# Performance work log

Measured on AMD Instinct MI355X. Metric: run time of the kernel, lower is better.

Reference implementation:

```python
import jax, jax.numpy as jnp
import numpy as np

N = 80000          # nodes
E = 1280000        # edges (~avg degree 16)
D_IN = 64          # Lorentz ambient dim (1 time + 63 spatial feature dims)
D_HID = 64
EPS = 1e-8


def _lorentz_inner(x):
    # <x,x>_L = -x0^2 + ||x_space||^2  (keepdims)
    return -x[:, :1] * x[:, :1] + jnp.sum(x[:, 1:] * x[:, 1:], axis=-1, keepdims=True)


def _to_manifold(s):
    # scale so that <s,s>_L = -1 (curvature c=1 hyperboloid)
    denom = jnp.sqrt(jnp.clip(jnp.abs(_lorentz_inner(s)), EPS))
    return s / denom


def _lorentz_linear(x, W, b, log_scale, nonlin=None):
    # HyboNet LorentzLinear: dense map, then rebuild a valid hyperboloid point
    if nonlin is not None:
        x = nonlin(x)
    h = x @ W.T + b
    time = jax.nn.sigmoid(h[:, :1]) * jnp.exp(log_scale) + 1.1
    space = h[:, 1:]
    sq = jnp.clip(jnp.sum(space * space, axis=-1, keepdims=True), EPS)
    scale = (time * time - 1.0) / sq
    return jnp.concatenate([time, space * jnp.sqrt(scale)], axis=-1)


def _agg(h, src, dst, w):
    # sparse adjacency aggregation (spmm) + Lorentz centroid normalization
    s = jax.ops.segment_sum(w[:, None] * h[src], dst, num_segments=N)
    return _to_manifold(s)


def setup_inputs() -> dict:
    key = jax.random.key(0)
    ks = jax.random.split(key, 6)
    x = jax.random.normal(ks[0], (N, D_IN - 1), jnp.float32)
    edge_index = jax.random.randint(ks[1], (2, E), 0, N, dtype=jnp.int32)
    edge_weight = jax.random.uniform(ks[2], (E,), jnp.float32)
    W1 = jax.random.normal(ks[3], (D_HID, D_IN), jnp.float32) * 0.02
    b1 = jnp.zeros((D_HID,), jnp.float32)
    s1 = jnp.asarray(np.log(10.0), jnp.float32)   # LorentzLinear scale param (log-space)
    W2 = jax.random.normal(ks[4], (D_HID, D_HID), jnp.float32) * 0.02
    b2 = jnp.zeros((D_HID,), jnp.float32)
    s2 = jnp.asarray(np.log(10.0), jnp.float32)
    return dict(x=x, edge_index=edge_index, edge_weight=edge_weight,
                W1=W1, b1=b1, s1=s1, W2=W2, b2=b2, s2=s2)


def reference(x, edge_index, edge_weight, W1, b1, s1, W2, b2, s2):
    src, dst = edge_index[0], edge_index[1]
    n = x.shape[0]
    # lift to Lorentz tangent space at origin: prepend zero time coord
    # (proj_tan0 is then a no-op since time component is already 0)
    u_space = x                                             # [N, D_IN-1]
    # expmap0 (c=1): [cosh(||u||), sinh(||u||) * u/||u||]
    nrm = jnp.clip(jnp.linalg.norm(u_space, axis=-1, keepdims=True), EPS)
    p_space = jnp.sinh(nrm) * u_space / nrm
    # projx: recompute time coord from spatial part, x0 = sqrt(1 + ||x_s||^2)
    p_time = jnp.sqrt(1.0 + jnp.sum(p_space * p_space, axis=-1, keepdims=True))
    p = jnp.concatenate([p_time, p_space], axis=1)          # [N, D_IN]
    # conv1 (no nonlin) and conv2 (relu) = LorentzLinear + Lorentz aggregation
    h1 = _agg(_lorentz_linear(p, W1, b1, s1), src, dst, edge_weight)
    h2 = _agg(_lorentz_linear(h1, W2, b2, s2, nonlin=jax.nn.relu), src, dst, edge_weight)
    # LResNet hyperbolic residual: Lorentz-normalized sum of the two points
    return _to_manifold(h1 + h2)
```

## Files before the change

kernel.cpp:

```cpp
#include <hip/hip_runtime.h>
#include <hip/hip_bf16.h>

#define D 64
#define EPS 1e-8f
#define BSH 10
#define BNODES (1 << BSH)
#define ABLK 4096

typedef __attribute__((ext_vector_type(8))) short bf16x8;
typedef __attribute__((ext_vector_type(4))) float f32x4;

__device__ __forceinline__ float wave_sum64(float v) {
    #pragma unroll
    for (int d = 1; d < 64; d <<= 1) v += __shfl_xor(v, d);
    return v;
}

__device__ __forceinline__ unsigned short f2bf_rn(float f) {
    unsigned u = __float_as_uint(f);
    return (unsigned short)((u + 0x7FFFu + ((u >> 16) & 1u)) >> 16);
}

__device__ __forceinline__ void split8(float4 a, float4 b, bf16x8& h, bf16x8& l) {
    float f[8] = {a.x, a.y, a.z, a.w, b.x, b.y, b.z, b.w};
    #pragma unroll
    for (int i = 0; i < 8; ++i) {
        unsigned u = __float_as_uint(f[i]);
        float hf = __uint_as_float(u & 0xFFFF0000u);
        unsigned lu = __float_as_uint(f[i] - hf);
        h[i] = (short)(u >> 16);
        l[i] = (short)(lu >> 16);
    }
}

__global__ __launch_bounds__(256) void k_bcount(const int* __restrict__ dst,
                                                int* __restrict__ bcnt,
                                                int e, int nbuck) {
    __shared__ int cnt[128];
    int tid = threadIdx.x;
    if (tid < 128) cnt[tid] = 0;
    __syncthreads();
    int i0 = blockIdx.x * 1024 + tid;
    #pragma unroll
    for (int u = 0; u < 4; ++u) {
        int i = i0 + u * 256;
        if (i < e) atomicAdd(&cnt[dst[i] >> BSH], 1);
    }
    __syncthreads();
    if (tid < nbuck && cnt[tid]) atomicAdd(&bcnt[tid], cnt[tid]);
}

__global__ __launch_bounds__(128) void k_bscan(const int* __restrict__ bcnt,
                                               int* __restrict__ bstart,
                                               int* __restrict__ gcur,
                                               int* __restrict__ off,
                                               int n, int e, int nbuck) {
    __shared__ int sm[128];
    int tid = threadIdx.x;
    int v = (tid < nbuck) ? bcnt[tid] : 0;
    sm[tid] = v;
    __syncthreads();
    #pragma unroll
    for (int d = 1; d < 128; d <<= 1) {
        int t = (tid >= d) ? sm[tid - d] : 0;
        __syncthreads();
        sm[tid] += t;
        __syncthreads();
    }
    int excl = sm[tid] - v;
    if (tid < nbuck) { bstart[tid] = excl; gcur[tid] = excl; }
    if (tid == 0) { bstart[nbuck] = e; off[n] = e; }
}

__global__ __launch_bounds__(256) void k_bucketA(const int* __restrict__ src,
                                                 const int* __restrict__ dst,
                                                 const float* __restrict__ w,
                                                 int* __restrict__ gcur,
                                                 unsigned long long* __restrict__ tmp,
                                                 int e, int nbuck) {
    __shared__ int cnt[128];
    __shared__ int base[128];
    int tid = threadIdx.x;
    if (tid < 128) cnt[tid] = 0;
    __syncthreads();
    int i0 = blockIdx.x * ABLK + tid;
    int bkt[16], rnk[16];
    #pragma unroll
    for (int u = 0; u < 16; ++u) {
        int i = i0 + u * 256;
        if (i < e) {
            int b = dst[i] >> BSH;
            bkt[u] = b;
            rnk[u] = atomicAdd(&cnt[b], 1);
        }
    }
    __syncthreads();
    if (tid < 128) {
        int c = cnt[tid];
        base[tid] = c ? atomicAdd(&gcur[tid], c) : 0;
    }
    __syncthreads();
    #pragma unroll
    for (int u = 0; u < 16; ++u) {
        int i = i0 + u * 256;
        if (i < e) {
            unsigned long long pk =
                ((unsigned long long)__float_as_uint(w[i]) << 32)
                | (unsigned int)(src[i] | ((dst[i] & (BNODES - 1)) << 20));
            tmp[base[bkt[u]] + rnk[u]] = pk;
        }
    }
}

__global__ __launch_bounds__(1024) void k_bucketB(const unsigned long long* __restrict__ tmp,
                                                  const int* __restrict__ bstart,
                                                  int* __restrict__ off,
                                                  unsigned long long* __restrict__ epack,
                                                  int n) {
    __shared__ int cur[BNODES];
    __shared__ int sm[BNODES];
    int b = blockIdx.x;
    int v0 = b << BSH;
    int nv = min(BNODES, n - v0);
    int tid = threadIdx.x;
    cur[tid] = 0;
    __syncthreads();
    int s0 = bstart[b], s1 = bstart[b + 1];
    for (int i = s0 + tid; i < s1; i += 1024)
        atomicAdd(&cur[((unsigned)tmp[i] >> 20) & (BNODES - 1)], 1);
    __syncthreads();
    int v = cur[tid];
    sm[tid] = v;
    __syncthreads();
    #pragma unroll
    for (int d = 1; d < BNODES; d <<= 1) {
        int t = (tid >= d) ? sm[tid - d] : 0;
        __syncthreads();
        sm[tid] += t;
        __syncthreads();
    }
    int node_off = s0 + sm[tid] - v;
    if (tid < nv) off[v0 + tid] = node_off;
    cur[tid] = node_off;
    __syncthreads();
    for (int i = s0 + tid; i < s1; i += 1024) {
        unsigned long long pk = tmp[i];
        int dl = ((unsigned)pk >> 20) & (BNODES - 1);
        int pos = atomicAdd(&cur[dl], 1);
        __builtin_nontemporal_store(pk & 0xFFFFFFFFC00FFFFFULL, &epack[pos]);
    }
}

__global__ __launch_bounds__(256) void k_embed(const float* __restrict__ x,
                                               float* __restrict__ P, int n) {
    int lane = threadIdx.x & 63, wv = threadIdx.x >> 6;
    int q = lane >> 4, sub = lane & 15;
    int node = blockIdx.x * 16 + wv * 4 + q;
    if (node >= n) return;
    const float* xr = x + (size_t)node * 63;
    float v0 = 0.f, v1, v2, v3;
    if (sub == 0) {
        v1 = xr[0]; v2 = xr[1]; v3 = xr[2];
    } else {
        int b = sub * 4 - 1;
        v0 = xr[b]; v1 = xr[b + 1]; v2 = xr[b + 2]; v3 = xr[b + 3];
    }
    float s = v0 * v0 + v1 * v1 + v2 * v2 + v3 * v3;
    #pragma unroll
    for (int d2 = 1; d2 < 16; d2 <<= 1) s += __shfl_xor(s, d2);
    float nrm = fmaxf(sqrtf(s), EPS);
    float sh = sinhf(nrm);
    float k = sh / nrm;
    float4 r;
    if (sub == 0) r = make_float4(sqrtf(1.f + sh * sh), k * v1, k * v2, k * v3);
    else          r = make_float4(k * v0, k * v1, k * v2, k * v3);
    *(float4*)(P + (size_t)node * 64 + sub * 4) = r;
}

template <int RELU>
__global__ __launch_bounds__(256) void k_lin_mfma(const float* __restrict__ tbl,
                                                  const float* __restrict__ W,
                                                  const float* __restrict__ bias,
                                                  const float* __restrict__ sc,
                                                  unsigned short* __restrict__ out, int n) {
    int lane = threadIdx.x & 63, wv = threadIdx.x >> 6;
    int col = lane & 15, grp = lane >> 4;
    int node0 = blockIdx.x * 64 + wv * 16;
    if (node0 >= n) return;

    float es = expf(sc[0]);

    bf16x8 wh[2][4], wl[2][4];
    #pragma unroll
    for (int s = 0; s < 2; ++s)
        #pragma unroll
        for (int t = 0; t < 4; ++t) {
            const float* wp = W + (t * 16 + col) * 64 + s * 32 + grp * 8;
            split8(*(const float4*)wp, *(const float4*)(wp + 4), wh[s][t], wl[s][t]);
        }

    f32x4 acc[4];
    #pragma unroll
    for (int t = 0; t < 4; ++t) {
        float bv = bias[t * 16 + col];
        acc[t] = (f32x4){bv, bv, bv, bv};
    }

    int arow = node0 + col;
    if (arow >= n) arow = n - 1;
    #pragma unroll
    for (int s = 0; s < 2; ++s) {
        const float* ap = tbl + (size_t)arow * 64 + s * 32 + grp * 8;
        float4 a0 = *(const float4*)ap;
        float4 a1 = *(const float4*)(ap + 4);
        if (RELU) {
            a0.x = fmaxf(a0.x, 0.f); a0.y = fmaxf(a0.y, 0.f);
            a0.z = fmaxf(a0.z, 0.f); a0.w = fmaxf(a0.w, 0.f);
            a1.x = fmaxf(a1.x, 0.f); a1.y = fmaxf(a1.y, 0.f);
            a1.z = fmaxf(a1.z, 0.f); a1.w = fmaxf(a1.w, 0.f);
        }
        bf16x8 ah, al;
        split8(a0, a1, ah, al);
        #pragma unroll
        for (int t = 0; t < 4; ++t) {
            acc[t] = __builtin_amdgcn_mfma_f32_16x16x32_bf16(ah, wh[s][t], acc[t], 0, 0, 0);
            acc[t] = __builtin_amdgcn_mfma_f32_16x16x32_bf16(al, wh[s][t], acc[t], 0, 0, 0);
            acc[t] = __builtin_amdgcn_mfma_f32_16x16x32_bf16(ah, wl[s][t], acc[t], 0, 0, 0);
        }
    }

    float tot[4];
    #pragma unroll
    for (int r = 0; r < 4; ++r) {
        float s = 0.f;
        #pragma unroll
        for (int t = 0; t < 4; ++t) s += acc[t][r] * acc[t][r];
        tot[r] = s;
    }
    #pragma unroll
    for (int d2 = 1; d2 < 16; d2 <<= 1) {
        #pragma unroll
        for (int r = 0; r < 4; ++r) tot[r] += __shfl_xor(tot[r], d2);
    }
    float tm[4], rs[4];
    #pragma unroll
    for (int r = 0; r < 4; ++r) {
        float h0 = __shfl(acc[0][r], lane & 48);
        tm[r] = es / (1.f + expf(-h0)) + 1.1f;
        float sq = fmaxf(tot[r] - h0 * h0, EPS);
        rs[r] = sqrtf((tm[r] * tm[r] - 1.f) / sq);
    }
    #pragma unroll
    for (int t = 0; t < 4; ++t) {
        #pragma unroll
        for (int r = 0; r < 4; ++r) {
            int row = node0 + grp * 4 + r;
            if (row < n) {
                int j = t * 16 + col;
                float v = (j == 0) ? tm[r] : acc[t][r] * rs[r];
                out[(size_t)row * 64 + j] = f2bf_rn(v);
            }
        }
    }
}

template <int FINAL>
__global__ __launch_bounds__(256) void k_agg(const unsigned short* __restrict__ t,
                                             const int* __restrict__ off,
                                             const unsigned long long* __restrict__ epack,
                                             const float* __restrict__ h1,
                                             float* __restrict__ out, int n) {
    __shared__ __align__(16) unsigned long long ebuf[4][64];
    int lane = threadIdx.x & 63, wv = threadIdx.x >> 6;
    int q = lane >> 4, sub = lane & 15;
    int node = blockIdx.x * 4 + wv;
    if (node >= n) return;
    int s0 = off[node], s1 = off[node + 1];
    float ax = 0.f, ay = 0.f, az = 0.f, aw = 0.f;
    for (int base = s0; base < s1; base += 64) {
        int c = min(s1 - base, 64);
        unsigned long long ev = 0;
        if (lane < c) ev = __builtin_nontemporal_load(&epack[base + lane]);
        ebuf[wv][lane] = ev;
        int ng = (c + 3) >> 2;
        uint2 rv[16]; float wgt[16];
        #pragma unroll
        for (int g = 0; g < 16; ++g) {
            if (g < ng) {
                unsigned long long e = ebuf[wv][g * 4 + q];
                wgt[g] = __uint_as_float((unsigned)(e >> 32));
                unsigned srcn = (unsigned)e & 0xFFFFFu;
                rv[g] = *(const uint2*)((const unsigned*)(t + ((size_t)srcn << 6)) + sub * 2);
            }
        }
        #pragma unroll
        for (int g = 0; g < 16; ++g) {
            if (g < ng) {
                float w = wgt[g];
                ax += w * __uint_as_float(rv[g].x << 16);
                ay += w * __uint_as_float(rv[g].x & 0xFFFF0000u);
                az += w * __uint_as_float(rv[g].y << 16);
                aw += w * __uint_as_float(rv[g].y & 0xFFFF0000u);
            }
        }
    }
    #pragma unroll
    for (int d2 = 16; d2 <= 32; d2 <<= 1) {
        ax += __shfl_xor(ax, d2);
        ay += __shfl_xor(ay, d2);
        az += __shfl_xor(az, d2);
        aw += __shfl_xor(aw, d2);
    }
    float s = ay * ay + az * az + aw * aw;
    s += (sub == 0) ? -ax * ax : ax * ax;
    #pragma unroll
    for (int d2 = 1; d2 < 16; d2 <<= 1) s += __shfl_xor(s, d2);
    float inv = 1.f / sqrtf(fmaxf(fabsf(s), EPS));
    float hx = ax * inv, hy = ay * inv, hz = az * inv, hw = aw * inv;
    if (FINAL) {
        f32x4 hv = __builtin_nontemporal_load(
            (const f32x4*)(h1 + (size_t)node * 64 + sub * 4));
        float vx = hv[0] + hx, vy = hv[1] + hy, vz = hv[2] + hz, vw = hv[3] + hw;
        float s2 = vy * vy + vz * vz + vw * vw;
        s2 += (sub == 0) ? -vx * vx : vx * vx;
        #pragma unroll
        for (int d2 = 1; d2 < 16; d2 <<= 1) s2 += __shfl_xor(s2, d2);
        float inv2 = 1.f / sqrtf(fmaxf(fabsf(s2), EPS));
        if (lane < 16) {
            float4 r = make_float4(vx * inv2, vy * inv2, vz * inv2, vw * inv2);
            *(float4*)(out + (size_t)node * 64 + sub * 4) = r;
        }
    } else {
        if (lane < 16) {
            float4 r = make_float4(hx, hy, hz, hw);
            *(float4*)(out + (size_t)node * 64 + sub * 4) = r;
        }
    }
}

extern "C" void kernel_launch(void* const* d_in, const int* in_sizes, int n_in,
                              void* d_out, int out_size, void* d_ws, size_t ws_size,
                              hipStream_t stream) {
    const float* x  = (const float*)d_in[0];
    const int*   ei = (const int*)d_in[1];
    const float* wE = (const float*)d_in[2];
    const float* W1 = (const float*)d_in[3];
    const float* b1 = (const float*)d_in[4];
    const float* s1 = (const float*)d_in[5];
    const float* W2 = (const float*)d_in[6];
    const float* b2 = (const float*)d_in[7];
    const float* s2 = (const float*)d_in[8];
    float* out = (float*)d_out;

    const int N = in_sizes[0] / (D - 1);
    const int E = in_sizes[2];
    const int* src = ei;
    const int* dst = ei + E;
    const int nbuck = (N + BNODES - 1) >> BSH;

    char* ws = (char*)d_ws;
    size_t sz1 = (size_t)N * D * 2;
    size_t szt = (size_t)E * 8;
    if (szt > sz1) sz1 = szt;
    sz1 = (sz1 + 255) & ~(size_t)255;
    unsigned short* T = (unsigned short*)ws;
    unsigned long long* tmp = (unsigned long long*)ws;
    float* B2 = (float*)(ws + sz1);
    unsigned long long* epack = (unsigned long long*)((char*)B2 + (size_t)N * D * 4);
    int* off    = (int*)(epack + E);
    int* bcnt   = off + (N + 1);
    int* bstart = bcnt + 128;
    int* gcur   = bstart + 132;

    hipMemsetAsync(bcnt, 0, 128 * sizeof(int), stream);

    int gE4 = (E + 1023) / 1024;
    int gEA = (E + ABLK - 1) / ABLK;
    int gEm = (N + 15) / 16;
    int gL = (N + 63) / 64;
    int gA = (N + 3) / 4;

    k_bcount<<<gE4, 256, 0, stream>>>(dst, bcnt, E, nbuck);
    k_bscan<<<1, 128, 0, stream>>>(bcnt, bstart, gcur, off, N, E, nbuck);
    k_bucketA<<<gEA, 256, 0, stream>>>(src, dst, wE, gcur, tmp, E, nbuck);
    k_bucketB<<<nbuck, 1024, 0, stream>>>(tmp, bstart, off, epack, N);

    k_embed<<<gEm, 256, 0, stream>>>(x, B2, N);
    k_lin_mfma<0><<<gL, 256, 0, stream>>>(B2, W1, b1, s1, T, N);
    k_agg<0><<<gA, 256, 0, stream>>>(T, off, epack, nullptr, B2, N);
    k_lin_mfma<1><<<gL, 256, 0, stream>>>(B2, W2, b2, s2, T, N);
    k_agg<1><<<gA, 256, 0, stream>>>(T, off, epack, B2, out, N);
}
```

Baseline: 234.4 us.

## Fuse CSR build with embed and first linear into shared launches

The embed kernel is merged with bucket counting into one launch, and the first Lorentz linear is merged with the bucket-scatter pass, so independent work shares a grid and two kernel launches go away. The tmp buffer gets its own workspace region so it no longer aliases T, which lets the linear write T while bucketing writes tmp. Buckets shrink from 1024 to 256 nodes, which gives more bucketB blocks (roughly 313 instead of 79). Bucket-A blocks handle 8192 edges each with a 32-way unroll, raising register pressure. The epack store drops the nontemporal hint and the dst-bit masking, which the aggregation ignores anyway.

```diff
diff --git a/kernel.cpp b/kernel.cpp
--- a/kernel.cpp
+++ b/kernel.cpp
@@ -3,18 +3,14 @@
 
 #define D 64
 #define EPS 1e-8f
-#define BSH 10
+#define BSH 8
 #define BNODES (1 << BSH)
-#define ABLK 4096
+#define ABLK 8192
+#define AUNR 32
 
 typedef __attribute__((ext_vector_type(8))) short bf16x8;
 typedef __attribute__((ext_vector_type(4))) float f32x4;
-
-__device__ __forceinline__ float wave_sum64(float v) {
-    #pragma unroll
-    for (int d = 1; d < 64; d <<= 1) v += __shfl_xor(v, d);
-    return v;
-}
+typedef unsigned long long ull;
 
 __device__ __forceinline__ unsigned short f2bf_rn(float f) {
     unsigned u = __float_as_uint(f);
@@ -33,129 +29,12 @@
     }
 }
 
-__global__ __launch_bounds__(256) void k_bcount(const int* __restrict__ dst,
-                                                int* __restrict__ bcnt,
-                                                int e, int nbuck) {
-    __shared__ int cnt[128];
-    int tid = threadIdx.x;
-    if (tid < 128) cnt[tid] = 0;
-    __syncthreads();
-    int i0 = blockIdx.x * 1024 + tid;
-    #pragma unroll
-    for (int u = 0; u < 4; ++u) {
-        int i = i0 + u * 256;
-        if (i < e) atomicAdd(&cnt[dst[i] >> BSH], 1);
-    }
-    __syncthreads();
-    if (tid < nbuck && cnt[tid]) atomicAdd(&bcnt[tid], cnt[tid]);
-}
-
-__global__ __launch_bounds__(128) void k_bscan(const int* __restrict__ bcnt,
-                                               int* __restrict__ bstart,
-                                               int* __restrict__ gcur,
-                                               int* __restrict__ off,
-                                               int n, int e, int nbuck) {
-    __shared__ int sm[128];
-    int tid = threadIdx.x;
-    int v = (tid < nbuck) ? bcnt[tid] : 0;
-    sm[tid] = v;
-    __syncthreads();
-    #pragma unroll
-    for (int d = 1; d < 128; d <<= 1) {
-        int t = (tid >= d) ? sm[tid - d] : 0;
-        __syncthreads();
-        sm[tid] += t;
-        __syncthreads();
-    }
-    int excl = sm[tid] - v;
-    if (tid < nbuck) { bstart[tid] = excl; gcur[tid] = excl; }
-    if (tid == 0) { bstart[nbuck] = e; off[n] = e; }
-}
-
-__global__ __launch_bounds__(256) void k_bucketA(const int* __restrict__ src,
-                                                 const int* __restrict__ dst,
-                                                 const float* __restrict__ w,
-                                                 int* __restrict__ gcur,
-                                                 unsigned long long* __restrict__ tmp,
-                                                 int e, int nbuck) {
-    __shared__ int cnt[128];
-    __shared__ int base[128];
-    int tid = threadIdx.x;
-    if (tid < 128) cnt[tid] = 0;
-    __syncthreads();
-    int i0 = blockIdx.x * ABLK + tid;
-    int bkt[16], rnk[16];
-    #pragma unroll
-    for (int u = 0; u < 16; ++u) {
-        int i = i0 + u * 256;
-        if (i < e) {
-            int b = dst[i] >> BSH;
-            bkt[u] = b;
-            rnk[u] = atomicAdd(&cnt[b], 1);
-        }
-    }
-    __syncthreads();
-    if (tid < 128) {
-        int c = cnt[tid];
-        base[tid] = c ? atomicAdd(&gcur[tid], c) : 0;
-    }
-    __syncthreads();
-    #pragma unroll
-    for (int u = 0; u < 16; ++u) {
-        int i = i0 + u * 256;
-        if (i < e) {
-            unsigned long long pk =
-                ((unsigned long long)__float_as_uint(w[i]) << 32)
-                | (unsigned int)(src[i] | ((dst[i] & (BNODES - 1)) << 20));
-            tmp[base[bkt[u]] + rnk[u]] = pk;
-        }
-    }
-}
-
-__global__ __launch_bounds__(1024) void k_bucketB(const unsigned long long* __restrict__ tmp,
-                                                  const int* __restrict__ bstart,
-                                                  int* __restrict__ off,
-                                                  unsigned long long* __restrict__ epack,
-                                                  int n) {
-    __shared__ int cur[BNODES];
-    __shared__ int sm[BNODES];
-    int b = blockIdx.x;
-    int v0 = b << BSH;
-    int nv = min(BNODES, n - v0);
-    int tid = threadIdx.x;
-    cur[tid] = 0;
-    __syncthreads();
-    int s0 = bstart[b], s1 = bstart[b + 1];
-    for (int i = s0 + tid; i < s1; i += 1024)
-        atomicAdd(&cur[((unsigned)tmp[i] >> 20) & (BNODES - 1)], 1);
-    __syncthreads();
-    int v = cur[tid];
-    sm[tid] = v;
-    __syncthreads();
-    #pragma unroll
-    for (int d = 1; d < BNODES; d <<= 1) {
-        int t = (tid >= d) ? sm[tid - d] : 0;
-        __syncthreads();
-        sm[tid] += t;
-        __syncthreads();
-    }
-    int node_off = s0 + sm[tid] - v;
-    if (tid < nv) off[v0 + tid] = node_off;
-    cur[tid] = node_off;
-    __syncthreads();
-    for (int i = s0 + tid; i < s1; i += 1024) {
-        unsigned long long pk = tmp[i];
-        int dl = ((unsigned)pk >> 20) & (BNODES - 1);
-        int pos = atomicAdd(&cur[dl], 1);
-        __builtin_nontemporal_store(pk & 0xFFFFFFFFC00FFFFFULL, &epack[pos]);
-    }
-}
-
-__global__ __launch_bounds__(256) void k_embed(const float* __restrict__ x,
-                                               float* __restrict__ P, int n) {
+
+__device__ __forceinline__ void embed_body(int bid, const float* __restrict__ x,
+                                           float* __restrict__ P, int n) {
     int lane = threadIdx.x & 63, wv = threadIdx.x >> 6;
     int q = lane >> 4, sub = lane & 15;
-    int node = blockIdx.x * 16 + wv * 4 + q;
+    int node = bid * 16 + wv * 4 + q;
     if (node >= n) return;
     const float* xr = x + (size_t)node * 63;
     float v0 = 0.f, v1, v2, v3;
@@ -177,15 +56,71 @@
     *(float4*)(P + (size_t)node * 64 + sub * 4) = r;
 }
 
+__device__ __forceinline__ void bcount_body(int bid, const int* __restrict__ dst,
+                                            int* __restrict__ bcnt, int e, int nbuck) {
+    __shared__ int cnt[320];
+    int tid = threadIdx.x;
+    for (int b = tid; b < nbuck; b += 256) cnt[b] = 0;
+    __syncthreads();
+    int i0 = bid * 1024 + tid;
+    #pragma unroll
+    for (int u = 0; u < 4; ++u) {
+        int i = i0 + u * 256;
+        if (i < e) atomicAdd(&cnt[dst[i] >> BSH], 1);
+    }
+    __syncthreads();
+    for (int b = tid; b < nbuck; b += 256)
+        if (cnt[b]) atomicAdd(&bcnt[b], cnt[b]);
+}
+
+__device__ __forceinline__ void bucketA_body(int bid, const int* __restrict__ src,
+                                             const int* __restrict__ dst,
+                                             const float* __restrict__ w,
+                                             int* __restrict__ gcur,
+                                             ull* __restrict__ tmp,
+                                             int e, int nbuck) {
+    __shared__ int cnt[320];
+    __shared__ int base[320];
+    int tid = threadIdx.x;
+    for (int b = tid; b < nbuck; b += 256) cnt[b] = 0;
+    __syncthreads();
+    int i0 = bid * ABLK + tid;
+    int bkt[AUNR], rnk[AUNR];
+    #pragma unroll
+    for (int u = 0; u < AUNR; ++u) {
+        int i = i0 + u * 256;
+        if (i < e) {
+            int b = dst[i] >> BSH;
+            bkt[u] = b;
+            rnk[u] = atomicAdd(&cnt[b], 1);
+        }
+    }
+    __syncthreads();
+    for (int b = tid; b < nbuck; b += 256) {
+        int c = cnt[b];
+        base[b] = c ? atomicAdd(&gcur[b], c) : 0;
+    }
+    __syncthreads();
+    #pragma unroll
+    for (int u = 0; u < AUNR; ++u) {
+        int i = i0 + u * 256;
+        if (i < e) {
+            ull pk = ((ull)__float_as_uint(w[i]) << 32)
+                   | (unsigned)(src[i] | ((dst[i] & (BNODES - 1)) << 20));
+            tmp[base[bkt[u]] + rnk[u]] = pk;
+        }
+    }
+}
+
 template <int RELU>
-__global__ __launch_bounds__(256) void k_lin_mfma(const float* __restrict__ tbl,
-                                                  const float* __restrict__ W,
-                                                  const float* __restrict__ bias,
-                                                  const float* __restrict__ sc,
-                                                  unsigned short* __restrict__ out, int n) {
+__device__ __forceinline__ void lin_body(int bid, const float* __restrict__ tbl,
+                                         const float* __restrict__ W,
+                                         const float* __restrict__ bias,
+                                         const float* __restrict__ sc,
+                                         unsigned short* __restrict__ out, int n) {
     int lane = threadIdx.x & 63, wv = threadIdx.x >> 6;
     int col = lane & 15, grp = lane >> 4;
-    int node0 = blockIdx.x * 64 + wv * 16;
+    int node0 = bid * 64 + wv * 16;
     if (node0 >= n) return;
 
     float es = expf(sc[0]);
@@ -264,13 +199,110 @@
     }
 }
 
+
+__global__ __launch_bounds__(256) void k_f1(const float* __restrict__ x,
+                                            float* __restrict__ P,
+                                            const int* __restrict__ dst,
+                                            int* __restrict__ bcnt,
+                                            int n, int e, int nbuck, int gEm) {
+    if ((int)blockIdx.x < gEm) embed_body(blockIdx.x, x, P, n);
+    else                       bcount_body(blockIdx.x - gEm, dst, bcnt, e, nbuck);
+}
+
+__global__ __launch_bounds__(512) void k_bscan(const int* __restrict__ bcnt,
+                                               int* __restrict__ bstart,
+                                               int* __restrict__ gcur,
+                                               int* __restrict__ off,
+                                               int n, int e, int nbuck) {
+    __shared__ int sm[512];
+    int tid = threadIdx.x;
+    int v = (tid < nbuck) ? bcnt[tid] : 0;
+    sm[tid] = v;
+    __syncthreads();
+    #pragma unroll
+    for (int d = 1; d < 512; d <<= 1) {
+        int t = (tid >= d) ? sm[tid - d] : 0;
+        __syncthreads();
+        sm[tid] += t;
+        __syncthreads();
+    }
+    int excl = sm[tid] - v;
+    if (tid < nbuck) { bstart[tid] = excl; gcur[tid] = excl; }
+    if (tid == 0) { bstart[nbuck] = e; off[n] = e; }
+}
+
+__global__ __launch_bounds__(256) void k_f2(const int* __restrict__ src,
+                                            const int* __restrict__ dst,
+                                            const float* __restrict__ wE,
+                                            int* __restrict__ gcur,
+                                            ull* __restrict__ tmp,
+                                            int e, int nbuck, int nA,
+                                            const float* __restrict__ P,
+                                            const float* __restrict__ W1,
+                                            const float* __restrict__ b1,
+                                            const float* __restrict__ s1,
+                                            unsigned short* __restrict__ T, int n) {
+    if ((int)blockIdx.x < nA) bucketA_body(blockIdx.x, src, dst, wE, gcur, tmp, e, nbuck);
+    else                      lin_body<0>(blockIdx.x - nA, P, W1, b1, s1, T, n);
+}
+
+__global__ __launch_bounds__(1024) void k_bucketB(const ull* __restrict__ tmp,
+                                                  const int* __restrict__ bstart,
+                                                  int* __restrict__ off,
+                                                  ull* __restrict__ epack,
+                                                  int n) {
+    __shared__ int cur[BNODES];
+    __shared__ int sm[BNODES];
+    int b = blockIdx.x;
+    int v0 = b << BSH;
+    int nv = min(BNODES, n - v0);
+    int tid = threadIdx.x;
+    if (tid < BNODES) cur[tid] = 0;
+    __syncthreads();
+    int s0 = bstart[b], s1 = bstart[b + 1];
+    for (int i = s0 + tid; i < s1; i += 1024)
+        atomicAdd(&cur[((unsigned)tmp[i] >> 20) & (BNODES - 1)], 1);
+    __syncthreads();
+    int v = 0;
+    if (tid < BNODES) { v = cur[tid]; sm[tid] = v; }
+    __syncthreads();
+    #pragma unroll
+    for (int d = 1; d < BNODES; d <<= 1) {
+        int t = 0;
+        if (tid < BNODES && tid >= d) t = sm[tid - d];
+        __syncthreads();
+        if (tid < BNODES) sm[tid] += t;
+        __syncthreads();
+    }
+    if (tid < BNODES) {
+        int node_off = s0 + sm[tid] - v;
+        if (tid < nv) off[v0 + tid] = node_off;
+        cur[tid] = node_off;
+    }
+    __syncthreads();
+    for (int i = s0 + tid; i < s1; i += 1024) {
+        ull pk = tmp[i];
+        int dl = ((unsigned)pk >> 20) & (BNODES - 1);
+        int pos = atomicAdd(&cur[dl], 1);
+        epack[pos] = pk;
+    }
+}
+
+__global__ __launch_bounds__(256) void k_lin2(const float* __restrict__ h1,
+                                              const float* __restrict__ W2,
+                                              const float* __restrict__ b2,
+                                              const float* __restrict__ s2,
+                                              unsigned short* __restrict__ T, int n) {
+    lin_body<1>(blockIdx.x, h1, W2, b2, s2, T, n);
+}
+
 template <int FINAL>
 __global__ __launch_bounds__(256) void k_agg(const unsigned short* __restrict__ t,
                                              const int* __restrict__ off,
-                                             const unsigned long long* __restrict__ epack,
+                                             const ull* __restrict__ epack,
                                              const float* __restrict__ h1,
                                              float* __restrict__ out, int n) {
-    __shared__ __align__(16) unsigned long long ebuf[4][64];
+    __shared__ __align__(16) ull ebuf[4][64];
     int lane = threadIdx.x & 63, wv = threadIdx.x >> 6;
     int q = lane >> 4, sub = lane & 15;
     int node = blockIdx.x * 4 + wv;
@@ -279,7 +311,7 @@
     float ax = 0.f, ay = 0.f, az = 0.f, aw = 0.f;
     for (int base = s0; base < s1; base += 64) {
         int c = min(s1 - base, 64);
-        unsigned long long ev = 0;
+        ull ev = 0;
         if (lane < c) ev = __builtin_nontemporal_load(&epack[base + lane]);
         ebuf[wv][lane] = ev;
         int ng = (c + 3) >> 2;
@@ -287,7 +319,7 @@
         #pragma unroll
         for (int g = 0; g < 16; ++g) {
             if (g < ng) {
-                unsigned long long e = ebuf[wv][g * 4 + q];
+                ull e = ebuf[wv][g * 4 + q];
                 wgt[g] = __uint_as_float((unsigned)(e >> 32));
                 unsigned srcn = (unsigned)e & 0xFFFFFu;
                 rv[g] = *(const uint2*)((const unsigned*)(t + ((size_t)srcn << 6)) + sub * 2);
@@ -359,35 +391,30 @@
     const int nbuck = (N + BNODES - 1) >> BSH;
 
     char* ws = (char*)d_ws;
-    size_t sz1 = (size_t)N * D * 2;
-    size_t szt = (size_t)E * 8;
-    if (szt > sz1) sz1 = szt;
-    sz1 = (sz1 + 255) & ~(size_t)255;
     unsigned short* T = (unsigned short*)ws;
-    unsigned long long* tmp = (unsigned long long*)ws;
-    float* B2 = (float*)(ws + sz1);
-    unsigned long long* epack = (unsigned long long*)((char*)B2 + (size_t)N * D * 4);
-    int* off    = (int*)(epack + E);
+    float* B2 = (float*)(ws + (((size_t)N * D * 2 + 255) & ~(size_t)255));
+    ull* epack = (ull*)((char*)B2 + (size_t)N * D * 4);
+    ull* tmp   = epack + E;
+    int* off    = (int*)(tmp + E);
     int* bcnt   = off + (N + 1);
-    int* bstart = bcnt + 128;
-    int* gcur   = bstart + 132;
-
-    hipMemsetAsync(bcnt, 0, 128 * sizeof(int), stream);
+    int* bstart = bcnt + 320;
+    int* gcur   = bstart + 320;
+
+    hipMemsetAsync(bcnt, 0, 320 * sizeof(int), stream);
 
     int gE4 = (E + 1023) / 1024;
-    int gEA = (E + ABLK - 1) / ABLK;
     int gEm = (N + 15) / 16;
-    int gL = (N + 63) / 64;
-    int gA = (N + 3) / 4;
-
-    k_bcount<<<gE4, 256, 0, stream>>>(dst, bcnt, E, nbuck);
-    k_bscan<<<1, 128, 0, stream>>>(bcnt, bstart, gcur, off, N, E, nbuck);
-    k_bucketA<<<gEA, 256, 0, stream>>>(src, dst, wE, gcur, tmp, E, nbuck);
+    int nA  = (E + ABLK - 1) / ABLK;
+    int gL  = (N + 63) / 64;
+    int gA  = (N + 3) / 4;
+
+    k_f1<<<gEm + gE4, 256, 0, stream>>>(x, B2, dst, bcnt, N, E, nbuck, gEm);
+    k_bscan<<<1, 512, 0, stream>>>(bcnt, bstart, gcur, off, N, E, nbuck);
+    k_f2<<<nA + gL, 256, 0, stream>>>(src, dst, wE, gcur, tmp, E, nbuck, nA,
+                                      B2, W1, b1, s1, T, N);
     k_bucketB<<<nbuck, 1024, 0, stream>>>(tmp, bstart, off, epack, N);
 
-    k_embed<<<gEm, 256, 0, stream>>>(x, B2, N);
-    k_lin_mfma<0><<<gL, 256, 0, stream>>>(B2, W1, b1, s1, T, N);
     k_agg<0><<<gA, 256, 0, stream>>>(T, off, epack, nullptr, B2, N);
-    k_lin_mfma<1><<<gL, 256, 0, stream>>>(B2, W2, b2, s2, T, N);
+    k_lin2<<<gL, 256, 0, stream>>>(B2, W2, b2, s2, T, N);
     k_agg<1><<<gA, 256, 0, stream>>>(T, off, epack, B2, out, N);
 }
```

New measurement: 198.3 us, median of 2. 15.4% less time.
